# Kernel optimization log

Measured on AMD Instinct MI355X. Metric: run time of the kernel, lower is better.

## Reference

```python
import jax, jax.numpy as jnp
import numpy as np

DIM = 8192
BATCH = 8

def setup_inputs() -> dict:
    key = jax.random.key(0)
    k1, k2 = jax.random.split(key)
    sdr = jax.random.normal(k1, (BATCH, DIM), dtype=jnp.float32)
    # scale synapse so sigmoid inputs stay in a reasonable range (weights clamped to [-1,1] in torch)
    synapse = jax.random.normal(k2, (DIM, DIM), dtype=jnp.float32) * (1.0 / np.sqrt(DIM))
    return {"sdr": sdr, "synapse": synapse, "steps": 2, "top_k": 60}

def reference(sdr, synapse, steps, top_k):
    # activation propagation: GEMV/GEMM -> sigmoid -> top-k sparsification per step
    act = sdr.astype(jnp.float32)
    B, N = act.shape
    rows = jnp.arange(B)[:, None]  # [B,1] row indices for scatter
    k = min(int(top_k), N)
    for _ in range(int(steps)):
        act = jax.nn.sigmoid(act @ synapse.T)          # [B,N]
        vals, idx = jax.lax.top_k(act, k)              # [B,k]
        act = jnp.zeros_like(act).at[rows, idx].set(vals)  # keep only top-k activations
    return act
```

## Files before the change

kernel.cpp:

```cpp
#include <hip/hip_runtime.h>
#include <cstdint>


#define DIM 8192
#define BATCH 8

__device__ __forceinline__ float sigmoidf_(float x) {
    return 1.0f / (1.0f + __expf(-x));
}

__global__ __launch_bounds__(256) void gemv8_sigmoid(
    const float* __restrict__ A,
    const float* __restrict__ W,
    float* __restrict__ Y)
{
    const int lane = threadIdx.x & 63;
    const int wid  = threadIdx.x >> 6;
    const int row0 = blockIdx.x * 4;
    const int jbeg = wid * (DIM / 4);
    const int jend = jbeg + (DIM / 4);
    const int jl   = lane * 4;

    float acc[4][8];
#pragma unroll
    for (int r = 0; r < 4; ++r)
#pragma unroll
        for (int b = 0; b < 8; ++b) acc[r][b] = 0.0f;

    for (int j0 = jbeg; j0 < jend; j0 += 256) {
        float4 a[8];
#pragma unroll
        for (int b = 0; b < 8; ++b)
            a[b] = *(const float4*)(A + b * DIM + j0 + jl);
        float4 wv[4];
#pragma unroll
        for (int r = 0; r < 4; ++r)
            wv[r] = *(const float4*)(W + (size_t)(row0 + r) * DIM + j0 + jl);
#pragma unroll
        for (int r = 0; r < 4; ++r) {
#pragma unroll
            for (int b = 0; b < 8; ++b) {
                acc[r][b] += wv[r].x * a[b].x;
                acc[r][b] += wv[r].y * a[b].y;
                acc[r][b] += wv[r].z * a[b].z;
                acc[r][b] += wv[r].w * a[b].w;
            }
        }
    }

    __shared__ float part[4][4][8];
#pragma unroll
    for (int r = 0; r < 4; ++r) {
#pragma unroll
        for (int b = 0; b < 8; ++b) {
            float v = acc[r][b];
#pragma unroll
            for (int off = 32; off > 0; off >>= 1)
                v += __shfl_down(v, off, 64);
            if (lane == 0) part[wid][r][b] = v;
        }
    }
    __syncthreads();

    if (threadIdx.x < 32) {
        const int r = threadIdx.x >> 3;
        const int b = threadIdx.x & 7;
        const float s = part[0][r][b] + part[1][r][b]
                      + part[2][r][b] + part[3][r][b];
        Y[b * DIM + row0 + r] = sigmoidf_(s);
    }
}

__global__ __launch_bounds__(256) void topk_sparsify(
    const float* __restrict__ Yin,
    float* __restrict__ Yout,
    const int* __restrict__ kptr)
{
    const int row  = blockIdx.x;
    const int tid  = threadIdx.x;
    const int lane = tid & 63;
    const int wid  = tid >> 6;
    int k = kptr ? *kptr : 60;
    if (k > DIM) k = DIM;

    uint32_t v[32];
    const float* src = Yin + (size_t)row * DIM;
#pragma unroll
    for (int i = 0; i < 32; ++i)
        v[i] = __float_as_uint(src[tid + i * 256]);

    __shared__ int s_part[4];
    __shared__ int s_ctr;

    uint32_t lo = 0u, hi = 0x3F800000u;
    while (hi - lo > 1u) {
        const uint32_t mid = lo + ((hi - lo) >> 1);
        int c = 0;
#pragma unroll
        for (int i = 0; i < 32; ++i) c += (v[i] >= mid) ? 1 : 0;
#pragma unroll
        for (int off = 32; off > 0; off >>= 1)
            c += __shfl_down(c, off, 64);
        if (lane == 0) s_part[wid] = c;
        __syncthreads();
        const int tot = s_part[0] + s_part[1] + s_part[2] + s_part[3];
        __syncthreads();
        if (tot >= k) lo = mid; else hi = mid;
    }
    const uint32_t cutoff = lo;

    int needg = 0;
    {
        int c = 0;
#pragma unroll
        for (int i = 0; i < 32; ++i) c += (v[i] > cutoff) ? 1 : 0;
#pragma unroll
        for (int off = 32; off > 0; off >>= 1)
            c += __shfl_down(c, off, 64);
        if (lane == 0) s_part[wid] = c;
        if (tid == 0) s_ctr = 0;
        __syncthreads();
        needg = s_part[0] + s_part[1] + s_part[2] + s_part[3];
    }
    const int need_eq = k - needg;

    float* dst = Yout + (size_t)row * DIM;
#pragma unroll
    for (int i = 0; i < 32; ++i) {
        const uint32_t b = v[i];
        float val = 0.0f;
        if (b > cutoff) {
            val = __uint_as_float(b);
        } else if (b == cutoff) {
            const int pos = atomicAdd(&s_ctr, 1);
            if (pos < need_eq) val = __uint_as_float(b);
        }
        dst[tid + i * 256] = val;
    }
}

extern "C" void kernel_launch(void* const* d_in, const int* in_sizes, int n_in,
                              void* d_out, int out_size, void* d_ws, size_t ws_size,
                              hipStream_t stream) {
    const float* sdr = (const float*)d_in[0];
    const float* syn = (const float*)d_in[1];
    const int* kptr  = (n_in > 3) ? (const int*)d_in[3] : nullptr;
    float* out = (float*)d_out;
    float* tmp = (float*)d_ws;

    gemv8_sigmoid<<<2048, 256, 0, stream>>>(sdr, syn, out);
    topk_sparsify<<<8, 256, 0, stream>>>(out, out, kptr);
    gemv8_sigmoid<<<2048, 256, 0, stream>>>(out, syn, tmp);
    topk_sparsify<<<8, 256, 0, stream>>>(tmp, out, kptr);
}
```

Before: 457.3 us.

## Widen GEMV row tile with register double-buffering; radix-histogram top-k select

```diff
diff --git a/kernel.cpp b/kernel.cpp
--- a/kernel.cpp
+++ b/kernel.cpp
@@ -16,59 +16,141 @@
 {
     const int lane = threadIdx.x & 63;
     const int wid  = threadIdx.x >> 6;
-    const int row0 = blockIdx.x * 4;
-    const int jbeg = wid * (DIM / 4);
-    const int jend = jbeg + (DIM / 4);
-    const int jl   = lane * 4;
-
-    float acc[4][8];
-#pragma unroll
-    for (int r = 0; r < 4; ++r)
+    const int row0 = blockIdx.x * 8;
+    const int jbeg = wid * (DIM / 4) + lane * 4;
+
+    const float* arow = A + jbeg;
+    const float* wrow[8];
+#pragma unroll
+    for (int r = 0; r < 8; ++r)
+        wrow[r] = W + (size_t)(row0 + r) * DIM + jbeg;
+
+    float4 a0[8], w0[8], a1[8], w1[8];
+#pragma unroll
+    for (int b = 0; b < 8; ++b) a0[b] = *(const float4*)(arow + (size_t)b * DIM);
+#pragma unroll
+    for (int r = 0; r < 8; ++r) w0[r] = *(const float4*)(wrow[r]);
+
+    float acc[8][8];
+#pragma unroll
+    for (int r = 0; r < 8; ++r)
 #pragma unroll
         for (int b = 0; b < 8; ++b) acc[r][b] = 0.0f;
 
-    for (int j0 = jbeg; j0 < jend; j0 += 256) {
-        float4 a[8];
-#pragma unroll
-        for (int b = 0; b < 8; ++b)
-            a[b] = *(const float4*)(A + b * DIM + j0 + jl);
-        float4 wv[4];
-#pragma unroll
-        for (int r = 0; r < 4; ++r)
-            wv[r] = *(const float4*)(W + (size_t)(row0 + r) * DIM + j0 + jl);
-#pragma unroll
-        for (int r = 0; r < 4; ++r) {
+#pragma unroll
+    for (int win = 0; win < 8; ++win) {
+        const int off = (win + 1) * 256;
+        if (win < 7) {
+#pragma unroll
+            for (int b = 0; b < 8; ++b)
+                a1[b] = *(const float4*)(arow + (size_t)b * DIM + off);
+#pragma unroll
+            for (int r = 0; r < 8; ++r)
+                w1[r] = *(const float4*)(wrow[r] + off);
+        }
+#pragma unroll
+        for (int r = 0; r < 8; ++r) {
 #pragma unroll
             for (int b = 0; b < 8; ++b) {
-                acc[r][b] += wv[r].x * a[b].x;
-                acc[r][b] += wv[r].y * a[b].y;
-                acc[r][b] += wv[r].z * a[b].z;
-                acc[r][b] += wv[r].w * a[b].w;
+                acc[r][b] += w0[r].x * a0[b].x;
+                acc[r][b] += w0[r].y * a0[b].y;
+                acc[r][b] += w0[r].z * a0[b].z;
+                acc[r][b] += w0[r].w * a0[b].w;
             }
         }
-    }
-
-    __shared__ float part[4][4][8];
-#pragma unroll
-    for (int r = 0; r < 4; ++r) {
+#pragma unroll
+        for (int b = 0; b < 8; ++b) a0[b] = a1[b];
+#pragma unroll
+        for (int r = 0; r < 8; ++r) w0[r] = w1[r];
+    }
+
+    __shared__ float part[4][8][8];
+#pragma unroll
+    for (int r = 0; r < 8; ++r) {
 #pragma unroll
         for (int b = 0; b < 8; ++b) {
             float v = acc[r][b];
 #pragma unroll
-            for (int off = 32; off > 0; off >>= 1)
-                v += __shfl_down(v, off, 64);
+            for (int o = 32; o > 0; o >>= 1)
+                v += __shfl_down(v, o, 64);
             if (lane == 0) part[wid][r][b] = v;
         }
     }
     __syncthreads();
 
-    if (threadIdx.x < 32) {
+    if (threadIdx.x < 64) {
         const int r = threadIdx.x >> 3;
         const int b = threadIdx.x & 7;
         const float s = part[0][r][b] + part[1][r][b]
                       + part[2][r][b] + part[3][r][b];
-        Y[b * DIM + row0 + r] = sigmoidf_(s);
-    }
+        Y[(size_t)b * DIM + row0 + r] = sigmoidf_(s);
+    }
+}
+
+
+__device__ __forceinline__ void scan_small(const int* hist, int nb, int k_need,
+                                           int lane, int* s_cut, int* s_gt)
+{
+    int running = 0;
+    for (int cb = nb - 64; cb >= 0; cb -= 64) {
+        const int b = cb + 63 - lane;
+        const int val = hist[b];
+        int c = val;
+#pragma unroll
+        for (int o = 1; o < 64; o <<= 1) {
+            const int u = __shfl_up(c, o, 64);
+            if (lane >= o) c += u;
+        }
+        const unsigned long long m = __ballot(running + c >= k_need);
+        if (m) {
+            const int f = (int)__ffsll(m) - 1;
+            const int cf = __shfl(c, f, 64);
+            const int vf = __shfl(val, f, 64);
+            if (lane == 0) { *s_cut = cb + 63 - f; *s_gt = running + cf - vf; }
+            return;
+        }
+        running += __shfl(c, 63, 64);
+    }
+    if (lane == 0) { *s_cut = 0; *s_gt = 0; }
+}
+
+__device__ __forceinline__ void scan_l1(const int* hist, const int* coarse,
+                                        int k_need, int lane,
+                                        int* s_cut, int* s_gt)
+{
+    int running = 0, seg = -1, segGT = 0;
+    for (int cb = 192; cb >= 0 && seg < 0; cb -= 64) {
+        const int b = cb + 63 - lane;
+        const int val = coarse[b];
+        int c = val;
+#pragma unroll
+        for (int o = 1; o < 64; o <<= 1) {
+            const int u = __shfl_up(c, o, 64);
+            if (lane >= o) c += u;
+        }
+        const unsigned long long m = __ballot(running + c >= k_need);
+        if (m) {
+            const int f = (int)__ffsll(m) - 1;
+            seg = cb + 63 - f;
+            segGT = running + __shfl(c, f, 64) - __shfl(val, f, 64);
+        } else {
+            running += __shfl(c, 63, 64);
+        }
+    }
+    if (seg < 0) seg = 0;
+    const int b = seg * 32 + 31 - lane;
+    const int val = (lane < 32) ? hist[b] : 0;
+    int c = val;
+#pragma unroll
+    for (int o = 1; o < 64; o <<= 1) {
+        const int u = __shfl_up(c, o, 64);
+        if (lane >= o) c += u;
+    }
+    const unsigned long long m = __ballot(segGT + c >= k_need);
+    const int f = (int)__ffsll(m) - 1;
+    const int cf = __shfl(c, f, 64);
+    const int vf = __shfl(val, f, 64);
+    if (lane == 0) { *s_cut = seg * 32 + 31 - f; *s_gt = segGT + cf - vf; }
 }
 
 __global__ __launch_bounds__(256) void topk_sparsify(
@@ -89,42 +171,61 @@
     for (int i = 0; i < 32; ++i)
         v[i] = __float_as_uint(src[tid + i * 256]);
 
-    __shared__ int s_part[4];
-    __shared__ int s_ctr;
-
-    uint32_t lo = 0u, hi = 0x3F800000u;
-    while (hi - lo > 1u) {
-        const uint32_t mid = lo + ((hi - lo) >> 1);
-        int c = 0;
-#pragma unroll
-        for (int i = 0; i < 32; ++i) c += (v[i] >= mid) ? 1 : 0;
-#pragma unroll
-        for (int off = 32; off > 0; off >>= 1)
-            c += __shfl_down(c, off, 64);
-        if (lane == 0) s_part[wid] = c;
-        __syncthreads();
-        const int tot = s_part[0] + s_part[1] + s_part[2] + s_part[3];
-        __syncthreads();
-        if (tot >= k) lo = mid; else hi = mid;
-    }
-    const uint32_t cutoff = lo;
-
-    int needg = 0;
+    float* dst = Yout + (size_t)row * DIM;
+    if (k <= 0) {
+#pragma unroll
+        for (int i = 0; i < 32; ++i) dst[tid + i * 256] = 0.0f;
+        return;
+    }
+
+    __shared__ int hist[8192];
+    __shared__ int coarse[256];
+    __shared__ int s_cut, s_gt, s_ctr;
+
+    for (int i = tid; i < 8192; i += 256) hist[i] = 0;
+    __syncthreads();
+#pragma unroll
+    for (int i = 0; i < 32; ++i) atomicAdd(&hist[v[i] >> 17], 1);
+    __syncthreads();
     {
-        int c = 0;
-#pragma unroll
-        for (int i = 0; i < 32; ++i) c += (v[i] > cutoff) ? 1 : 0;
-#pragma unroll
-        for (int off = 32; off > 0; off >>= 1)
-            c += __shfl_down(c, off, 64);
-        if (lane == 0) s_part[wid] = c;
-        if (tid == 0) s_ctr = 0;
-        __syncthreads();
-        needg = s_part[0] + s_part[1] + s_part[2] + s_part[3];
-    }
-    const int need_eq = k - needg;
-
-    float* dst = Yout + (size_t)row * DIM;
+        int s = 0;
+        const int base = tid * 32;
+        for (int i = 0; i < 32; ++i) s += hist[base + i];
+        coarse[tid] = s;
+    }
+    __syncthreads();
+    if (wid == 0) scan_l1(hist, coarse, k, lane, &s_cut, &s_gt);
+    __syncthreads();
+    const uint32_t cut1 = (uint32_t)s_cut;
+    const int gt1 = s_gt;
+
+    for (int i = tid; i < 512; i += 256) hist[i] = 0;
+    __syncthreads();
+#pragma unroll
+    for (int i = 0; i < 32; ++i)
+        if ((v[i] >> 17) == cut1) atomicAdd(&hist[(v[i] >> 8) & 0x1FF], 1);
+    __syncthreads();
+    if (wid == 0) scan_small(hist, 512, k - gt1, lane, &s_cut, &s_gt);
+    __syncthreads();
+    const uint32_t cut2 = (uint32_t)s_cut;
+    const int gt2 = s_gt;
+
+    const uint32_t pref = (cut1 << 9) | cut2;
+    for (int i = tid; i < 256; i += 256) hist[i] = 0;
+    if (tid == 0) s_ctr = 0;
+    __syncthreads();
+#pragma unroll
+    for (int i = 0; i < 32; ++i)
+        if ((v[i] >> 8) == pref) atomicAdd(&hist[v[i] & 0xFF], 1);
+    __syncthreads();
+    if (wid == 0) scan_small(hist, 256, k - gt1 - gt2, lane, &s_cut, &s_gt);
+    __syncthreads();
+    const uint32_t cut3 = (uint32_t)s_cut;
+    const int gt3 = s_gt;
+
+    const uint32_t cutoff  = (pref << 8) | cut3;
+    const int      need_eq = k - (gt1 + gt2 + gt3);
+
 #pragma unroll
     for (int i = 0; i < 32; ++i) {
         const uint32_t b = v[i];
@@ -148,8 +249,8 @@
     float* out = (float*)d_out;
     float* tmp = (float*)d_ws;
 
-    gemv8_sigmoid<<<2048, 256, 0, stream>>>(sdr, syn, out);
+    gemv8_sigmoid<<<1024, 256, 0, stream>>>(sdr, syn, out);
     topk_sparsify<<<8, 256, 0, stream>>>(out, out, kptr);
-    gemv8_sigmoid<<<2048, 256, 0, stream>>>(out, syn, tmp);
+    gemv8_sigmoid<<<1024, 256, 0, stream>>>(out, syn, tmp);
     topk_sparsify<<<8, 256, 0, stream>>>(tmp, out, kptr);
 }
```

Result: slower. 626.4 us (+37.0%).
